# Optimization experiments

Hardware: AMD Instinct MI355X
Metric: run time of the kernel (lower is better)

## Reference

```python
import jax, jax.numpy as jnp
import numpy as np

N, E, IN, H, D = 50000, 800000, 128, 2, 64  # nodes, edges, in_dim, heads, out_dim per head
EPS = 1e-16  # PyG softmax denominator epsilon


def setup_inputs() -> dict:
    key = jax.random.key(0)
    ks = jax.random.split(key, 10)
    s = 1.0 / np.sqrt(IN)
    u = lambda k, shape: jax.random.uniform(k, shape, jnp.float32, -s, s)
    return {
        "x": jax.random.normal(ks[0], (N, IN), jnp.float32),
        "edge_index": jax.random.randint(ks[1], (2, E), 0, N, jnp.int64),
        "Wq": u(ks[2], (IN, H * D)), "bq": u(ks[3], (H * D,)),
        "Wk": u(ks[4], (IN, H * D)), "bk": u(ks[5], (H * D,)),
        "Wv": u(ks[6], (IN, H * D)), "bv": u(ks[7], (H * D,)),
        "Ws": u(ks[8], (IN, H * D)), "bs": u(ks[9], (H * D,)),
    }


def reference(x, edge_index, Wq, bq, Wk, bk, Wv, bv, Ws, bs):
    src, dst = edge_index[0], edge_index[1]
    # node-level projections [N, H, D]
    q = (x @ Wq + bq).reshape(N, H, D)
    k = (x @ Wk + bk).reshape(N, H, D)
    v = (x @ Wv + bv).reshape(N, H, D)
    # per-edge attention logits [E, H]
    alpha = jnp.einsum('ehd,ehd->eh', q[dst], k[src]) / np.float32(np.sqrt(D))
    # segment softmax over incoming edges of each dst node
    amax = jax.ops.segment_max(alpha, dst, num_segments=N)      # [N, H]
    amax = jnp.where(jnp.isfinite(amax), amax, 0.0)
    ealpha = jnp.exp(alpha - amax[dst])                          # [E, H]
    denom = jax.ops.segment_sum(ealpha, dst, num_segments=N)     # [N, H]
    w = ealpha / (denom[dst] + EPS)                              # [E, H]
    # scatter-aggregate weighted values -> [N, H, D]
    agg = jax.ops.segment_sum(w[:, :, None] * v[src], dst, num_segments=N)
    out = agg.reshape(N, H * D) + (x @ Ws + bs)                  # root/skip term
    return jax.nn.relu(out)
```

## Files before the change

kernel.cpp:

```cpp
#include <hip/hip_runtime.h>
#include <hip/hip_bf16.h>


#define N_NODES 50000
#define E_EDGES 800000
#define IN_DIM  128
#define HD      128
#define NPB     256
#define NB      196
#define EB      2048
#define NBLK_AC ((E_EDGES + EB - 1) / EB)
#define NTILES  ((N_NODES + 63) / 64)
#define PBLK    256
#define PSCALE  0.18033688011112042f

typedef float  f32x4  __attribute__((ext_vector_type(4)));
typedef float  f32x2  __attribute__((ext_vector_type(2)));
typedef __bf16 bf16x8 __attribute__((ext_vector_type(8)));
typedef unsigned short u16x8 __attribute__((ext_vector_type(8)));

__device__ __forceinline__ float bf2f(unsigned short u) {
    return __uint_as_float((unsigned int)u << 16);
}

__global__ __launch_bounds__(512) void proj_kernel(
    const float* __restrict__ x,
    const float* __restrict__ Wq, const float* __restrict__ bq,
    const float* __restrict__ Wk, const float* __restrict__ bk,
    const float* __restrict__ Wv, const float* __restrict__ bv,
    const float* __restrict__ Ws, const float* __restrict__ bs,
    __bf16* __restrict__ qb, unsigned char* __restrict__ kv8,
    __bf16* __restrict__ sbuf)
{
    __shared__ __bf16 xs[64][136];

    const int tid  = threadIdx.x;
    const int lane = tid & 63;
    const int wave = tid >> 6;
    const int l15  = lane & 15;
    const int g    = lane >> 4;

    const int p    = wave >> 1;
    const int colh = (wave & 1) * 64;
    const float* Wp     = (p == 0) ? Wq : (p == 1) ? Wk : (p == 2) ? Wv : Ws;
    const float* bias_p = (p == 0) ? bq : (p == 1) ? bk : (p == 2) ? bv : bs;

    bf16x8 Bf[4][4];
    #pragma unroll
    for (int ks = 0; ks < 4; ++ks) {
        #pragma unroll
        for (int cf = 0; cf < 4; ++cf) {
            bf16x8 b;
            #pragma unroll
            for (int j = 0; j < 8; ++j)
                b[j] = (__bf16)Wp[(size_t)(ks * 32 + g * 8 + j) * HD + colh + cf * 16 + l15];
            Bf[ks][cf] = b;
        }
    }

    float bias_v[4];
    #pragma unroll
    for (int cf = 0; cf < 4; ++cf) bias_v[cf] = bias_p[colh + cf * 16 + l15];

    const int srow = tid >> 5;
    const int sc4  = tid & 31;

    int t = blockIdx.x;
    float4 pre[4];
    if (t < NTILES) {
        #pragma unroll
        for (int it = 0; it < 4; ++it) {
            int row  = it * 16 + srow;
            int grow = t * 64 + row;
            pre[it] = (grow < N_NODES) ? *(const float4*)(x + (size_t)grow * IN_DIM + sc4 * 4)
                                       : make_float4(0.f, 0.f, 0.f, 0.f);
        }
    }

    for (; t < NTILES; t += PBLK) {
        __syncthreads();
        #pragma unroll
        for (int it = 0; it < 4; ++it) {
            int row = it * 16 + srow;
            __bf16* dst = &xs[row][sc4 * 4];
            dst[0] = (__bf16)pre[it].x; dst[1] = (__bf16)pre[it].y;
            dst[2] = (__bf16)pre[it].z; dst[3] = (__bf16)pre[it].w;
        }
        __syncthreads();

        int tn = t + PBLK;
        if (tn < NTILES) {
            #pragma unroll
            for (int it = 0; it < 4; ++it) {
                int row  = it * 16 + srow;
                int grow = tn * 64 + row;
                pre[it] = (grow < N_NODES) ? *(const float4*)(x + (size_t)grow * IN_DIM + sc4 * 4)
                                           : make_float4(0.f, 0.f, 0.f, 0.f);
            }
        }

        f32x4 acc[4][4];
        #pragma unroll
        for (int i = 0; i < 4; ++i)
            #pragma unroll
            for (int j = 0; j < 4; ++j) acc[i][j] = (f32x4){0.f, 0.f, 0.f, 0.f};

        #pragma unroll
        for (int ks = 0; ks < 4; ++ks) {
            #pragma unroll
            for (int rf = 0; rf < 4; ++rf) {
                bf16x8 A = *(const bf16x8*)&xs[rf * 16 + l15][ks * 32 + g * 8];
                #pragma unroll
                for (int cf = 0; cf < 4; ++cf)
                    acc[rf][cf] = __builtin_amdgcn_mfma_f32_16x16x32_bf16(A, Bf[ks][cf], acc[rf][cf], 0, 0, 0);
            }
        }

        const int nodebase = t * 64;
        if (p == 0 || p == 3) {
            __bf16* outp = (p == 0) ? qb : sbuf;
            #pragma unroll
            for (int cf = 0; cf < 4; ++cf) {
                int col = colh + cf * 16 + l15;
                #pragma unroll
                for (int rf = 0; rf < 4; ++rf) {
                    #pragma unroll
                    for (int r = 0; r < 4; ++r) {
                        int grow = nodebase + rf * 16 + g * 4 + r;
                        if (grow < N_NODES)
                            outp[(size_t)grow * HD + col] = (__bf16)(acc[rf][cf][r] + bias_v[cf]);
                    }
                }
            }
        } else {
            unsigned char* outp = kv8 + ((p == 2) ? 128 : 0);
            #pragma unroll
            for (int cf = 0; cf < 4; ++cf) {
                int col = colh + cf * 16 + l15;
                #pragma unroll
                for (int rf = 0; rf < 4; ++rf) {
                    #pragma unroll
                    for (int r = 0; r < 4; ++r) {
                        int grow = nodebase + rf * 16 + g * 4 + r;
                        if (grow < N_NODES) {
                            float val = acc[rf][cf][r] + bias_v[cf];
                            unsigned int pk = __builtin_amdgcn_cvt_pk_fp8_f32(val, val, 0, false);
                            outp[(size_t)grow * 256 + col] = (unsigned char)(pk & 0xff);
                        }
                    }
                }
            }
        }
    }
}

__global__ __launch_bounds__(256) void histA(
    const int* __restrict__ ei, int* __restrict__ hist)
{
    __shared__ int h[NB];
    const int tid = threadIdx.x;
    for (int i = tid; i < NB; i += 256) h[i] = 0;
    __syncthreads();

    const int* dsts = ei + E_EDGES;
    const int base = blockIdx.x * EB;
    #pragma unroll
    for (int half = 0; half < 2; ++half) {
        int e0 = base + half * 1024 + tid * 4;
        if (e0 + 3 < E_EDGES) {
            int4 d = *(const int4*)(dsts + e0);
            atomicAdd(&h[d.x >> 8], 1);
            atomicAdd(&h[d.y >> 8], 1);
            atomicAdd(&h[d.z >> 8], 1);
            atomicAdd(&h[d.w >> 8], 1);
        } else {
            for (int j = 0; j < 4; ++j)
                if (e0 + j < E_EDGES) atomicAdd(&h[dsts[e0 + j] >> 8], 1);
        }
    }
    __syncthreads();
    for (int i = tid; i < NB; i += 256)
        hist[i * NBLK_AC + blockIdx.x] = h[i];
}

__global__ __launch_bounds__(256) void scanB1(
    int* __restrict__ hist, int* __restrict__ sums)
{
    __shared__ int a[512];
    const int tid = threadIdx.x;
    const int b   = blockIdx.x;
    int* hb = hist + (size_t)b * NBLK_AC;

    a[tid]       = (tid       < NBLK_AC) ? hb[tid]       : 0;
    a[tid + 256] = (tid + 256 < NBLK_AC) ? hb[tid + 256] : 0;
    __syncthreads();
    #pragma unroll
    for (int d = 1; d < 512; d <<= 1) {
        int v0 = a[tid],       u0 = (tid       >= d) ? a[tid - d]       : 0;
        int v1 = a[tid + 256], u1 = (tid + 256 >= d) ? a[tid + 256 - d] : 0;
        __syncthreads();
        a[tid] = v0 + u0; a[tid + 256] = v1 + u1;
        __syncthreads();
    }
    if (tid < NBLK_AC)       hb[tid]       = (tid == 0) ? 0 : a[tid - 1];
    if (tid + 256 < NBLK_AC) hb[tid + 256] = a[tid + 255];
    if (tid == 0) sums[b] = a[NBLK_AC - 1];
}

__global__ __launch_bounds__(256) void scanB2(
    const int* __restrict__ sums, int* __restrict__ binbase)
{
    __shared__ int a[256];
    const int tid = threadIdx.x;
    a[tid] = (tid < NB) ? sums[tid] : 0;
    __syncthreads();
    #pragma unroll
    for (int d = 1; d < 256; d <<= 1) {
        int v = a[tid];
        int u = (tid >= d) ? a[tid - d] : 0;
        __syncthreads();
        a[tid] = v + u;
        __syncthreads();
    }
    if (tid < NB) binbase[tid] = (tid == 0) ? 0 : a[tid - 1];
    if (tid == 0) binbase[NB] = a[NB - 1] + 0;
    if (tid == 0) binbase[NB] = a[255];
}

__global__ __launch_bounds__(256) void scatterC(
    const int* __restrict__ ei, const int* __restrict__ hist,
    const int* __restrict__ binbase, int2* __restrict__ part)
{
    __shared__ int hb[NB];
    __shared__ int h2[NB];
    const int tid = threadIdx.x;
    for (int i = tid; i < NB; i += 256) {
        hb[i] = hist[i * NBLK_AC + blockIdx.x] + binbase[i];
        h2[i] = 0;
    }
    __syncthreads();

    const int* srcs = ei;
    const int* dsts = ei + E_EDGES;
    const int base = blockIdx.x * EB;
    #pragma unroll
    for (int half = 0; half < 2; ++half) {
        int e0 = base + half * 1024 + tid * 4;
        if (e0 + 3 < E_EDGES) {
            int4 s4 = *(const int4*)(srcs + e0);
            int4 d4 = *(const int4*)(dsts + e0);
            int bin, r;
            bin = d4.x >> 8; r = atomicAdd(&h2[bin], 1); part[hb[bin] + r] = make_int2(s4.x, d4.x);
            bin = d4.y >> 8; r = atomicAdd(&h2[bin], 1); part[hb[bin] + r] = make_int2(s4.y, d4.y);
            bin = d4.z >> 8; r = atomicAdd(&h2[bin], 1); part[hb[bin] + r] = make_int2(s4.z, d4.z);
            bin = d4.w >> 8; r = atomicAdd(&h2[bin], 1); part[hb[bin] + r] = make_int2(s4.w, d4.w);
        } else {
            for (int j = 0; j < 4; ++j) {
                if (e0 + j < E_EDGES) {
                    int sv = srcs[e0 + j], dv = dsts[e0 + j];
                    int bin = dv >> 8;
                    int r = atomicAdd(&h2[bin], 1);
                    part[hb[bin] + r] = make_int2(sv, dv);
                }
            }
        }
    }
}

__global__ __launch_bounds__(256) void buildD(
    const int2* __restrict__ part, const int* __restrict__ binbase,
    int* __restrict__ slot, int* __restrict__ nbase)
{
    __shared__ int cnt2[NPB];
    __shared__ int pfx[NPB];
    __shared__ int ofs[NPB];
    const int tid = threadIdx.x;
    const int b   = blockIdx.x;
    const int lo  = binbase[b];
    const int hi  = binbase[b + 1];
    const int n0  = b * NPB;

    cnt2[tid] = 0;
    __syncthreads();
    for (int i = lo + tid; i < hi; i += 256)
        atomicAdd(&cnt2[part[i].y - n0], 1);
    __syncthreads();

    pfx[tid] = cnt2[tid];
    __syncthreads();
    #pragma unroll
    for (int d = 1; d < NPB; d <<= 1) {
        int v = pfx[tid];
        int u = (tid >= d) ? pfx[tid - d] : 0;
        __syncthreads();
        pfx[tid] = v + u;
        __syncthreads();
    }
    const int excl = pfx[tid] - cnt2[tid];
    ofs[tid] = excl;
    const int node = n0 + tid;
    if (node < N_NODES) nbase[node] = lo + excl;
    if (b == NB - 1 && tid == 0) nbase[N_NODES] = E_EDGES;
    __syncthreads();

    for (int i = lo + tid; i < hi; i += 256) {
        int2 e = part[i];
        int r = atomicAdd(&ofs[e.y - n0], 1);
        slot[lo + r] = e.x;
    }
}

__global__ __launch_bounds__(256) void aggregate_kernel(
    const __bf16* __restrict__ qb, const unsigned char* __restrict__ kv8,
    const __bf16* __restrict__ sbuf,
    const int* __restrict__ nbase, const int* __restrict__ slot,
    float* __restrict__ out)
{
    const int tid  = threadIdx.x;
    const int lane = tid & 63;
    const int wave = tid >> 6;
    const int h    = lane >> 5;
    const int lh   = lane & 31;
    const int s    = lh >> 4;
    const int l16  = lh & 15;
    const int node = blockIdx.x * 8 + wave * 2 + h;
    const bool nvalid = node < N_NODES;
    const int nc = nvalid ? node : 0;

    const int bse = nbase[nc];
    const int deg = nvalid ? (nbase[nc + 1] - bse) : 0;

    u16x8 qu = *(const u16x8*)(qb + (size_t)nc * HD + 8 * l16);
    float qf[8];
    #pragma unroll
    for (int c = 0; c < 8; ++c) qf[c] = bf2f(qu[c]);

    int my_src = (lh < deg) ? slot[bse + lh] : 0;

    float lsum = 0.f;
    float acc[8];
    #pragma unroll
    for (int c = 0; c < 8; ++c) acc[c] = 0.f;

    const int sbase = h * 32;
    for (int i = 0; i < deg; i += 8) {
        int  jj[4], se[4];
        uint2 kr[4], vr[4];
        float d[4];

        #pragma unroll
        for (int r = 0; r < 4; ++r) {
            jj[r] = i + 2 * r + s;
            int sv = __shfl(my_src, sbase + (jj[r] & 31), 64);
            if (jj[r] >= 32) sv = slot[bse + jj[r]];
            se[r] = (jj[r] < deg) ? sv : 0;
        }
        #pragma unroll
        for (int r = 0; r < 4; ++r) {
            const unsigned char* rowp = kv8 + (size_t)se[r] * 256 + 8 * l16;
            kr[r] = *(const uint2*)rowp;
            vr[r] = *(const uint2*)(rowp + 128);
        }
        #pragma unroll
        for (int r = 0; r < 4; ++r) {
            f32x2 ka = __builtin_amdgcn_cvt_pk_f32_fp8(kr[r].x, 0);
            f32x2 kb_ = __builtin_amdgcn_cvt_pk_f32_fp8(kr[r].x, 1);
            f32x2 kc = __builtin_amdgcn_cvt_pk_f32_fp8(kr[r].y, 0);
            f32x2 kd = __builtin_amdgcn_cvt_pk_f32_fp8(kr[r].y, 1);
            d[r] = qf[0] * ka.x + qf[1] * ka.y + qf[2] * kb_.x + qf[3] * kb_.y
                 + qf[4] * kc.x + qf[5] * kc.y + qf[6] * kd.x + qf[7] * kd.y;
        }
        #pragma unroll
        for (int m = 1; m <= 4; m <<= 1) {
            d[0] += __shfl_xor(d[0], m);
            d[1] += __shfl_xor(d[1], m);
            d[2] += __shfl_xor(d[2], m);
            d[3] += __shfl_xor(d[3], m);
        }
        #pragma unroll
        for (int r = 0; r < 4; ++r) {
            float a2 = (jj[r] < deg) ? d[r] * PSCALE : -INFINITY;
            float p  = exp2f(a2);
            lsum += p;
            f32x2 va = __builtin_amdgcn_cvt_pk_f32_fp8(vr[r].x, 0);
            f32x2 vb_ = __builtin_amdgcn_cvt_pk_f32_fp8(vr[r].x, 1);
            f32x2 vc = __builtin_amdgcn_cvt_pk_f32_fp8(vr[r].y, 0);
            f32x2 vd = __builtin_amdgcn_cvt_pk_f32_fp8(vr[r].y, 1);
            acc[0] += p * va.x;  acc[1] += p * va.y;
            acc[2] += p * vb_.x; acc[3] += p * vb_.y;
            acc[4] += p * vc.x;  acc[5] += p * vc.y;
            acc[6] += p * vd.x;  acc[7] += p * vd.y;
        }
    }

    lsum += __shfl_xor(lsum, 16);
    #pragma unroll
    for (int c = 0; c < 8; ++c) acc[c] += __shfl_xor(acc[c], 16);

    float inv = (deg > 0) ? 1.f / (lsum + 1e-16f) : 0.f;
    u16x8 su = *(const u16x8*)(sbuf + (size_t)nc * HD + 8 * l16);

    f32x4 ov;
    #pragma unroll
    for (int cc = 0; cc < 4; ++cc) {
        float av;
        unsigned short sv;
        switch (cc) {
            case 0: av = s ? acc[4] : acc[0]; sv = s ? su[4] : su[0]; break;
            case 1: av = s ? acc[5] : acc[1]; sv = s ? su[5] : su[1]; break;
            case 2: av = s ? acc[6] : acc[2]; sv = s ? su[6] : su[2]; break;
            default: av = s ? acc[7] : acc[3]; sv = s ? su[7] : su[3]; break;
        }
        ov[cc] = fmaxf(av * inv + bf2f(sv), 0.f);
    }
    if (nvalid)
        *(f32x4*)(out + (size_t)node * HD + 8 * l16 + 4 * s) = ov;
}

extern "C" void kernel_launch(void* const* d_in, const int* in_sizes, int n_in,
                              void* d_out, int out_size, void* d_ws, size_t ws_size,
                              hipStream_t stream)
{
    const float* x  = (const float*)d_in[0];
    const int*   ei = (const int*)d_in[1];
    const float* Wq = (const float*)d_in[2];
    const float* bq = (const float*)d_in[3];
    const float* Wk = (const float*)d_in[4];
    const float* bk = (const float*)d_in[5];
    const float* Wv = (const float*)d_in[6];
    const float* bv = (const float*)d_in[7];
    const float* Ws = (const float*)d_in[8];
    const float* bs = (const float*)d_in[9];

    char* ws = (char*)d_ws;
    size_t off = 0;
    auto alloc = [&](size_t bytes) {
        void* p = ws + off;
        off += (bytes + 255) & ~(size_t)255;
        return p;
    };
    const size_t projB = (size_t)N_NODES * HD * sizeof(__bf16);
    __bf16* qb = (__bf16*)alloc(projB);
    unsigned char* kv8 = (unsigned char*)alloc((size_t)N_NODES * 256);
    __bf16* sbf = (__bf16*)alloc(projB);
    int* hist    = (int*)alloc((size_t)NB * NBLK_AC * sizeof(int));
    int* sums    = (int*)alloc((size_t)NB * sizeof(int));
    int* binbase = (int*)alloc((size_t)(NB + 1) * sizeof(int));
    int2* part   = (int2*)alloc((size_t)E_EDGES * sizeof(int2));
    int* slot    = (int*)alloc((size_t)E_EDGES * sizeof(int));
    int* nbase   = (int*)alloc((size_t)(N_NODES + 1) * sizeof(int));

    histA<<<NBLK_AC, 256, 0, stream>>>(ei, hist);
    scanB1<<<NB, 256, 0, stream>>>(hist, sums);
    scanB2<<<1, 256, 0, stream>>>(sums, binbase);
    scatterC<<<NBLK_AC, 256, 0, stream>>>(ei, hist, binbase, part);
    buildD<<<NB, 256, 0, stream>>>(part, binbase, slot, nbase);

    proj_kernel<<<PBLK, 512, 0, stream>>>(
        x, Wq, bq, Wk, bk, Wv, bv, Ws, bs, qb, kv8, sbf);

    aggregate_kernel<<<(N_NODES + 7) / 8, 256, 0, stream>>>(
        qb, kv8, sbf, nbase, slot, (float*)d_out);
}
```

Baseline: 91.97 us.

## Transpose MFMA operands for vectorized projection stores, double proj grid, direct slot loads

The projection kernel swaps the MFMA A/B operands so each lane holds four consecutive output columns of one node. This lets q/s results go out as packed 8-byte bf16 stores and k/v results as packed 4-byte fp8 stores, where before each lane wrote scattered single elements. The projection grid also doubles from 256 to 512 blocks. In the aggregation kernel, the register-cached source list plus shuffle is replaced by direct loads from the slot array, which simplifies the code but adds memory traffic.

```diff
diff --git a/kernel.cpp b/kernel.cpp
--- a/kernel.cpp
+++ b/kernel.cpp
@@ -11,12 +11,13 @@
 #define EB      2048
 #define NBLK_AC ((E_EDGES + EB - 1) / EB)
 #define NTILES  ((N_NODES + 63) / 64)
-#define PBLK    256
+#define PBLK    512
 #define PSCALE  0.18033688011112042f
 
 typedef float  f32x4  __attribute__((ext_vector_type(4)));
 typedef float  f32x2  __attribute__((ext_vector_type(2)));
 typedef __bf16 bf16x8 __attribute__((ext_vector_type(8)));
+typedef unsigned short u16x4 __attribute__((ext_vector_type(4)));
 typedef unsigned short u16x8 __attribute__((ext_vector_type(8)));
 
 __device__ __forceinline__ float bf2f(unsigned short u) {
@@ -58,9 +59,12 @@
         }
     }
 
-    float bias_v[4];
-    #pragma unroll
-    for (int cf = 0; cf < 4; ++cf) bias_v[cf] = bias_p[colh + cf * 16 + l15];
+    float bias_v[4][4];
+    #pragma unroll
+    for (int cf = 0; cf < 4; ++cf)
+        #pragma unroll
+        for (int j = 0; j < 4; ++j)
+            bias_v[cf][j] = bias_p[colh + cf * 16 + g * 4 + j];
 
     const int srow = tid >> 5;
     const int sc4  = tid & 31;
@@ -112,7 +116,7 @@
                 bf16x8 A = *(const bf16x8*)&xs[rf * 16 + l15][ks * 32 + g * 8];
                 #pragma unroll
                 for (int cf = 0; cf < 4; ++cf)
-                    acc[rf][cf] = __builtin_amdgcn_mfma_f32_16x16x32_bf16(A, Bf[ks][cf], acc[rf][cf], 0, 0, 0);
+                    acc[rf][cf] = __builtin_amdgcn_mfma_f32_16x16x32_bf16(Bf[ks][cf], A, acc[rf][cf], 0, 0, 0);
             }
         }
 
@@ -120,33 +124,36 @@
         if (p == 0 || p == 3) {
             __bf16* outp = (p == 0) ? qb : sbuf;
             #pragma unroll
-            for (int cf = 0; cf < 4; ++cf) {
-                int col = colh + cf * 16 + l15;
-                #pragma unroll
-                for (int rf = 0; rf < 4; ++rf) {
+            for (int rf = 0; rf < 4; ++rf) {
+                int grow = nodebase + rf * 16 + l15;
+                if (grow < N_NODES) {
                     #pragma unroll
-                    for (int r = 0; r < 4; ++r) {
-                        int grow = nodebase + rf * 16 + g * 4 + r;
-                        if (grow < N_NODES)
-                            outp[(size_t)grow * HD + col] = (__bf16)(acc[rf][cf][r] + bias_v[cf]);
+                    for (int cf = 0; cf < 4; ++cf) {
+                        u16x4 pk;
+                        #pragma unroll
+                        for (int j = 0; j < 4; ++j) {
+                            __bf16 b = (__bf16)(acc[rf][cf][j] + bias_v[cf][j]);
+                            pk[j] = __builtin_bit_cast(unsigned short, b);
+                        }
+                        *(u16x4*)(outp + (size_t)grow * HD + colh + cf * 16 + g * 4) = pk;
                     }
                 }
             }
         } else {
             unsigned char* outp = kv8 + ((p == 2) ? 128 : 0);
             #pragma unroll
-            for (int cf = 0; cf < 4; ++cf) {
-                int col = colh + cf * 16 + l15;
-                #pragma unroll
-                for (int rf = 0; rf < 4; ++rf) {
+            for (int rf = 0; rf < 4; ++rf) {
+                int grow = nodebase + rf * 16 + l15;
+                if (grow < N_NODES) {
                     #pragma unroll
-                    for (int r = 0; r < 4; ++r) {
-                        int grow = nodebase + rf * 16 + g * 4 + r;
-                        if (grow < N_NODES) {
-                            float val = acc[rf][cf][r] + bias_v[cf];
-                            unsigned int pk = __builtin_amdgcn_cvt_pk_fp8_f32(val, val, 0, false);
-                            outp[(size_t)grow * 256 + col] = (unsigned char)(pk & 0xff);
-                        }
+                    for (int cf = 0; cf < 4; ++cf) {
+                        float v0 = acc[rf][cf][0] + bias_v[cf][0];
+                        float v1 = acc[rf][cf][1] + bias_v[cf][1];
+                        float v2 = acc[rf][cf][2] + bias_v[cf][2];
+                        float v3 = acc[rf][cf][3] + bias_v[cf][3];
+                        unsigned int w = __builtin_amdgcn_cvt_pk_fp8_f32(v0, v1, 0, false);
+                        w = __builtin_amdgcn_cvt_pk_fp8_f32(v2, v3, w, true);
+                        *(unsigned int*)(outp + (size_t)grow * 256 + colh + cf * 16 + g * 4) = w;
                     }
                 }
             }
@@ -223,7 +230,6 @@
         __syncthreads();
     }
     if (tid < NB) binbase[tid] = (tid == 0) ? 0 : a[tid - 1];
-    if (tid == 0) binbase[NB] = a[NB - 1] + 0;
     if (tid == 0) binbase[NB] = a[255];
 }
 
@@ -335,14 +341,11 @@
     #pragma unroll
     for (int c = 0; c < 8; ++c) qf[c] = bf2f(qu[c]);
 
-    int my_src = (lh < deg) ? slot[bse + lh] : 0;
-
     float lsum = 0.f;
     float acc[8];
     #pragma unroll
     for (int c = 0; c < 8; ++c) acc[c] = 0.f;
 
-    const int sbase = h * 32;
     for (int i = 0; i < deg; i += 8) {
         int  jj[4], se[4];
         uint2 kr[4], vr[4];
@@ -351,8 +354,7 @@
         #pragma unroll
         for (int r = 0; r < 4; ++r) {
             jj[r] = i + 2 * r + s;
-            int sv = __shfl(my_src, sbase + (jj[r] & 31), 64);
-            if (jj[r] >= 32) sv = slot[bse + jj[r]];
+            int sv = slot[bse + ((jj[r] < deg) ? jj[r] : 0)];
             se[r] = (jj[r] < deg) ? sv : 0;
         }
         #pragma unroll
```

Result: slower. 98.54 us (+7.2%).
